# Performance work log

Measured on AMD Instinct MI355X. Metric: run time of the kernel, lower is better.

Reference implementation:

```python
import math
import jax, jax.numpy as jnp
import numpy as np

HEADS = 9
EMBED = 32
TEMPERATURE = 3000.0

def _conv1x1(x, W, b):
    # x: [B,C,H,W], W: [O,C], b: [O]  (1x1 conv == channel matmul)
    return jnp.einsum('bchw,oc->bohw', x, W) + b[None, :, None, None]

def setup_inputs() -> dict:
    key = jax.random.key(0)
    ks = jax.random.split(key, 14)
    B, H, W = 2, 64, 64
    h2, w2 = 32, 32
    hd = HEADS * EMBED  # 288
    s = 0.1
    return {
        'second_frame': jax.random.normal(ks[0], (B, 3, H, W), jnp.float32),
        'first_frame_aligned': jax.random.normal(ks[1], (B, 3, H, W), jnp.float32),
        'second_frame_feat': jax.random.normal(ks[2], (B, 4, h2, w2), jnp.float32),
        'first_frame_feat_aligned': jax.random.normal(ks[3], (B, 4, h2, w2), jnp.float32),
        'Wq': jax.random.normal(ks[4], (hd, 3), jnp.float32) * s,
        'bq': jax.random.normal(ks[5], (hd,), jnp.float32) * s,
        'Wk': jax.random.normal(ks[6], (hd, 3), jnp.float32) * s,
        'bk': jax.random.normal(ks[7], (hd,), jnp.float32) * s,
        'Wv': jax.random.normal(ks[8], (hd, 4), jnp.float32) * s,
        'bv': jax.random.normal(ks[9], (hd,), jnp.float32) * s,
        'Wp': jax.random.normal(ks[10], (4, hd), jnp.float32) * s,
        'bp': jax.random.normal(ks[11], (4,), jnp.float32) * s,
        'Wt': jax.random.normal(ks[12], (1, EMBED), jnp.float32) * s,
        'bt': jax.random.normal(ks[13], (1,), jnp.float32) * s,
    }

def reference(second_frame, first_frame_aligned, second_frame_feat,
              first_frame_feat_aligned, Wq, bq, Wk, bk, Wv, bv, Wp, bp, Wt, bt):
    B, _, H, W = second_frame.shape
    HW = H * W
    # bilinear upsample of aligned features to (H, W); half-pixel centers == align_corners=False
    feat_up = jax.image.resize(first_frame_feat_aligned,
                               (B, first_frame_feat_aligned.shape[1], H, W),
                               method='linear', antialias=False)
    Q = _conv1x1(second_frame, Wq, bq).reshape(B, HEADS, EMBED, HW)
    K = _conv1x1(first_frame_aligned, Wk, bk).reshape(B, HEADS, EMBED, HW)
    V = _conv1x1(feat_up, Wv, bv).reshape(B, HEADS, EMBED, HW)
    Qn = jnp.transpose(Q, (0, 1, 3, 2))                      # [B,h,HW,d]
    sim = jnp.einsum('bhnd,bhdm->bhnm', Qn, K) / math.sqrt(EMBED)  # [B,h,HW,HW]
    # learned per-query threshold from Q
    t = jnp.einsum('bhnd,od->bhno', Qn, Wt) + bt             # [B,h,HW,1]
    attn = jax.nn.relu((sim - t) / TEMPERATURE)              # no row normalization
    out = jnp.einsum('bhnm,bhdm->bhnd', attn, V)             # [B,h,HW,d]
    out = jnp.transpose(out, (0, 1, 3, 2)).reshape(B, HEADS * EMBED, H, W)
    out_feat = _conv1x1(out, Wp, bp)                         # [B,4,H,W]
    h2, w2 = second_frame_feat.shape[-2:]
    out_feat_down = jax.image.resize(out_feat, (B, out_feat.shape[1], h2, w2),
                                     method='linear', antialias=False)
    final_feat = second_frame_feat + out_feat_down
    return final_feat, out_feat_down
```

## Files before the change

kernel.cpp:

```cpp
#include <hip/hip_runtime.h>
#include <hip/hip_bf16.h>
#include <cstddef>

#define NHEADS 9
#define D 32
#define SQ 4096
#define ZSPLIT 4
#define MBLK (SQ / ZSPLIT)
#define CHUNKS (MBLK / 64)
#define KROW 40
#define VROW 70

typedef __attribute__((ext_vector_type(8))) short bf16x8;
typedef __attribute__((ext_vector_type(4))) short bf16x4;
typedef __attribute__((ext_vector_type(4))) float f32x4;

__device__ __forceinline__ unsigned int f2bf(float f) {
    unsigned int u = __float_as_uint(f);
    u += 0x7fffu + ((u >> 16) & 1u);
    return u >> 16;
}

__device__ __forceinline__ unsigned int cvt_pk_bf16(float a, float b) {
#if __has_builtin(__builtin_amdgcn_cvt_pk_bf16_f32)
    typedef __attribute__((ext_vector_type(2))) __bf16 bf2;
    union { bf2 v; unsigned int u; } cv;
    cv.v = __builtin_amdgcn_cvt_pk_bf16_f32(a, b);
    return cv.u;
#else
    return (f2bf(b) << 16) | f2bf(a);
#endif
}

__device__ __forceinline__ bf16x4 relu_pack(f32x4 st) {
    float a0 = fmaxf(st[0], 0.0f);
    float a1 = fmaxf(st[1], 0.0f);
    float a2 = fmaxf(st[2], 0.0f);
    float a3 = fmaxf(st[3], 0.0f);
    union { unsigned int u[2]; bf16x4 v; } r;
    r.u[0] = cvt_pk_bf16(a0, a1);
    r.u[1] = cvt_pk_bf16(a2, a3);
    return r.v;
}

__global__ __launch_bounds__(256) void prep_kernel(
    const float* __restrict__ x2, const float* __restrict__ x1,
    const float* __restrict__ feat1,
    const float* __restrict__ Wq, const float* __restrict__ bq,
    const float* __restrict__ Wk, const float* __restrict__ bk,
    const float* __restrict__ Wv, const float* __restrict__ bv,
    const float* __restrict__ Wt, const float* __restrict__ bt,
    unsigned short* __restrict__ Qb, unsigned short* __restrict__ Kb,
    unsigned short* __restrict__ Vb, float* __restrict__ tbuf,
    float* __restrict__ of)
{
    int idx = blockIdx.x * blockDim.x + threadIdx.x;
    if (idx < 2 * 4 * SQ) of[idx] = 0.0f;
    int g  = idx & 3;
    int n  = (idx >> 2) & (SQ - 1);
    int bh = idx >> 14;
    int h  = bh % NHEADS;
    int b  = bh / NHEADS;

    float xs0 = x2[((size_t)b * 3 + 0) * SQ + n];
    float xs1 = x2[((size_t)b * 3 + 1) * SQ + n];
    float xs2 = x2[((size_t)b * 3 + 2) * SQ + n];
    float ys0 = x1[((size_t)b * 3 + 0) * SQ + n];
    float ys1 = x1[((size_t)b * 3 + 1) * SQ + n];
    float ys2 = x1[((size_t)b * 3 + 2) * SQ + n];

    int yy = n >> 6, xx = n & 63;
    int jy = yy >> 1, jx = xx >> 1;
    int j0, j1, i0, i1; float wy0, wy1, wx0, wx1;
    if (yy & 1) { j0 = jy; j1 = (jy < 31) ? jy + 1 : 31; wy0 = 0.75f; wy1 = 0.25f; }
    else        { j0 = (jy > 0) ? jy - 1 : 0; j1 = jy;   wy0 = 0.25f; wy1 = 0.75f; }
    if (xx & 1) { i0 = jx; i1 = (jx < 31) ? jx + 1 : 31; wx0 = 0.75f; wx1 = 0.25f; }
    else        { i0 = (jx > 0) ? jx - 1 : 0; i1 = jx;   wx0 = 0.25f; wx1 = 0.75f; }

    float fu[4];
#pragma unroll
    for (int c = 0; c < 4; ++c) {
        const float* f = feat1 + ((size_t)b * 4 + c) * 1024;
        fu[c] = wy0 * (wx0 * f[j0 * 32 + i0] + wx1 * f[j0 * 32 + i1]) +
                wy1 * (wx0 * f[j1 * 32 + i0] + wx1 * f[j1 * 32 + i1]);
    }

    const int d0 = g * 8;
    unsigned int qp[4], kp[4], vp[4];
    float tpart = 0.0f;
#pragma unroll
    for (int j = 0; j < 8; ++j) {
        int d = d0 + j, hd = h * D + d;
        float q = bq[hd] + Wq[hd * 3] * xs0 + Wq[hd * 3 + 1] * xs1 + Wq[hd * 3 + 2] * xs2;
        float k = bk[hd] + Wk[hd * 3] * ys0 + Wk[hd * 3 + 1] * ys1 + Wk[hd * 3 + 2] * ys2;
        float v = bv[hd] + Wv[hd * 4] * fu[0] + Wv[hd * 4 + 1] * fu[1] +
                  Wv[hd * 4 + 2] * fu[2] + Wv[hd * 4 + 3] * fu[3];
        tpart += q * Wt[d];
        unsigned int qb_ = f2bf(q), kb_ = f2bf(k), vb_ = f2bf(v);
        if (j & 1) { qp[j >> 1] |= qb_ << 16; kp[j >> 1] |= kb_ << 16; vp[j >> 1] |= vb_ << 16; }
        else       { qp[j >> 1]  = qb_;       kp[j >> 1]  = kb_;       vp[j >> 1]  = vb_; }
    }
    tpart += __shfl_xor(tpart, 1);
    tpart += __shfl_xor(tpart, 2);
    if (g == 0) tbuf[(size_t)bh * SQ + n] = tpart + bt[0];

    size_t base = ((size_t)bh * SQ + n) * D + d0;
    *(uint4*)(Qb + base) = make_uint4(qp[0], qp[1], qp[2], qp[3]);
    *(uint4*)(Kb + base) = make_uint4(kp[0], kp[1], kp[2], kp[3]);
    *(uint4*)(Vb + base) = make_uint4(vp[0], vp[1], vp[2], vp[3]);
}

__global__ __launch_bounds__(256, 4) void attn_kernel(
    const unsigned short* __restrict__ Qb,
    const unsigned short* __restrict__ Kb,
    const unsigned short* __restrict__ Vb,
    const float* __restrict__ tbuf,
    const float* __restrict__ Wp,
    float* __restrict__ of)
{
    __shared__ __align__(16) unsigned short Ks[64 * KROW];
    __shared__ __align__(16) unsigned short Vs[32 * VROW];

    const int bh   = blockIdx.y;
    const int h    = bh % NHEADS;
    const int b    = bh / NHEADS;
    const int n0   = blockIdx.x * 256;
    const int mc0  = blockIdx.z * MBLK;
    const int tid  = threadIdx.x;
    const int wave = tid >> 6;
    const int lane = tid & 63;
    const int l15  = lane & 15;
    const int quad = lane >> 4;

    const int nw = n0 + wave * 64;

    const unsigned short* qbase = Qb + ((size_t)bh * SQ + nw + l15) * D + quad * 8;
    bf16x8 qfA = *(const bf16x8*)(qbase);
    bf16x8 qfB = *(const bf16x8*)(qbase + 16 * D);
    bf16x8 qfC = *(const bf16x8*)(qbase + 32 * D);
    bf16x8 qfD = *(const bf16x8*)(qbase + 48 * D);

    const float SQRT32 = 5.656854249492381f;
    const float* tb = tbuf + (size_t)bh * SQ + nw + l15;
    float TA = tb[0]  * SQRT32;
    float TB = tb[16] * SQRT32;
    float TC = tb[32] * SQRT32;
    float TD = tb[48] * SQRT32;
    const f32x4 ciA = {-TA, -TA, -TA, -TA};
    const f32x4 ciB = {-TB, -TB, -TB, -TB};
    const f32x4 ciC = {-TC, -TC, -TC, -TC};
    const f32x4 ciD = {-TD, -TD, -TD, -TD};

    const uint4* Kg4 = (const uint4*)(Kb + (size_t)bh * SQ * D);
    const uint4* Vg4 = (const uint4*)(Vb + (size_t)bh * SQ * D);

    const int krow = tid >> 2;
    const int kcol = (tid & 3) * 8;
    unsigned short* kdst = Ks + krow * KROW + kcol;
    unsigned short* vdst = Vs + kcol * VROW + krow;

    f32x4 accAl = {0.f,0.f,0.f,0.f}, accAh = {0.f,0.f,0.f,0.f};
    f32x4 accBl = {0.f,0.f,0.f,0.f}, accBh = {0.f,0.f,0.f,0.f};
    f32x4 accCl = {0.f,0.f,0.f,0.f}, accCh = {0.f,0.f,0.f,0.f};
    f32x4 accDl = {0.f,0.f,0.f,0.f}, accDh = {0.f,0.f,0.f,0.f};

    uint4 kreg = Kg4[(size_t)mc0 * 4 + tid];
    uint4 vreg = Vg4[(size_t)mc0 * 4 + tid];

    for (int c = 0; c < CHUNKS; ++c) {
        __syncthreads();
        *(uint4*)kdst = kreg;
        {
            union { uint4 u; unsigned short s[8]; } vv; vv.u = vreg;
#pragma unroll
            for (int j = 0; j < 8; ++j) vdst[j * VROW] = vv.s[j];
        }
        kreg = Kg4[(size_t)(mc0 + (c + 1) * 64) * 4 + tid];
        vreg = Vg4[(size_t)(mc0 + (c + 1) * 64) * 4 + tid];
        __syncthreads();

#pragma unroll
        for (int s = 0; s < 4; ++s) {
            bf16x8 kf = *(const bf16x8*)(Ks + (s * 16 + l15) * KROW + quad * 8);
            bf16x4 va = *(const bf16x4*)(Vs + l15 * VROW + s * 16 + quad * 4);
            bf16x4 vb = *(const bf16x4*)(Vs + (l15 + 16) * VROW + s * 16 + quad * 4);

            f32x4 stA = __builtin_amdgcn_mfma_f32_16x16x32_bf16(kf, qfA, ciA, 0, 0, 0);
            f32x4 stB = __builtin_amdgcn_mfma_f32_16x16x32_bf16(kf, qfB, ciB, 0, 0, 0);
            f32x4 stC = __builtin_amdgcn_mfma_f32_16x16x32_bf16(kf, qfC, ciC, 0, 0, 0);
            f32x4 stD = __builtin_amdgcn_mfma_f32_16x16x32_bf16(kf, qfD, ciD, 0, 0, 0);

            bf16x4 pA = relu_pack(stA);
            bf16x4 pB = relu_pack(stB);
            bf16x4 pC = relu_pack(stC);
            bf16x4 pD = relu_pack(stD);

            accAl = __builtin_amdgcn_mfma_f32_16x16x16bf16_1k(va, pA, accAl, 0, 0, 0);
            accAh = __builtin_amdgcn_mfma_f32_16x16x16bf16_1k(vb, pA, accAh, 0, 0, 0);
            accBl = __builtin_amdgcn_mfma_f32_16x16x16bf16_1k(va, pB, accBl, 0, 0, 0);
            accBh = __builtin_amdgcn_mfma_f32_16x16x16bf16_1k(vb, pB, accBh, 0, 0, 0);
            accCl = __builtin_amdgcn_mfma_f32_16x16x16bf16_1k(va, pC, accCl, 0, 0, 0);
            accCh = __builtin_amdgcn_mfma_f32_16x16x16bf16_1k(vb, pC, accCh, 0, 0, 0);
            accDl = __builtin_amdgcn_mfma_f32_16x16x16bf16_1k(va, pD, accDl, 0, 0, 0);
            accDh = __builtin_amdgcn_mfma_f32_16x16x16bf16_1k(vb, pD, accDh, 0, 0, 0);
        }
    }

    const float s1 = 5.892556509887896e-05f;
    const float* wph = Wp + h * D + quad * 4;
#pragma unroll
    for (int o = 0; o < 4; ++o) {
        float cA = 0.f, cB = 0.f, cC = 0.f, cD = 0.f;
#pragma unroll
        for (int r = 0; r < 4; ++r) {
            float wlo = wph[o * 288 + r], whi = wph[o * 288 + 16 + r];
            cA += accAl[r] * wlo + accAh[r] * whi;
            cB += accBl[r] * wlo + accBh[r] * whi;
            cC += accCl[r] * wlo + accCh[r] * whi;
            cD += accDl[r] * wlo + accDh[r] * whi;
        }
        cA += __shfl_xor(cA, 16); cA += __shfl_xor(cA, 32);
        cB += __shfl_xor(cB, 16); cB += __shfl_xor(cB, 32);
        cC += __shfl_xor(cC, 16); cC += __shfl_xor(cC, 32);
        cD += __shfl_xor(cD, 16); cD += __shfl_xor(cD, 32);
        if (quad == 0) {
            float* ob = &of[((size_t)b * 4 + o) * SQ + nw + l15];
            atomicAdd(ob,      cA * s1);
            atomicAdd(ob + 16, cB * s1);
            atomicAdd(ob + 32, cC * s1);
            atomicAdd(ob + 48, cD * s1);
        }
    }
}

__global__ void final_kernel(const float* __restrict__ of,
                             const float* __restrict__ sff,
                             const float* __restrict__ bp,
                             float* __restrict__ dout)
{
    int tid = blockIdx.x * blockDim.x + threadIdx.x;
    if (tid >= 8192) return;
    int i  = tid & 31;
    int jj = (tid >> 5) & 31;
    int bo = tid >> 10;
    int o  = bo & 3;
    const float* src = of + (size_t)bo * SQ;
    int y = jj * 2, x = i * 2;
    float dval = 0.25f * (src[y * 64 + x] + src[y * 64 + x + 1] +
                          src[(y + 1) * 64 + x] + src[(y + 1) * 64 + x + 1]) + bp[o];
    dout[tid]        = sff[tid] + dval;
    dout[8192 + tid] = dval;
}

extern "C" void kernel_launch(void* const* d_in, const int* in_sizes, int n_in,
                              void* d_out, int out_size, void* d_ws, size_t ws_size,
                              hipStream_t stream)
{
    const float* second_frame = (const float*)d_in[0];
    const float* first_frame  = (const float*)d_in[1];
    const float* sff          = (const float*)d_in[2];
    const float* ffa          = (const float*)d_in[3];
    const float* Wq = (const float*)d_in[4];
    const float* bq = (const float*)d_in[5];
    const float* Wk = (const float*)d_in[6];
    const float* bk = (const float*)d_in[7];
    const float* Wv = (const float*)d_in[8];
    const float* bv = (const float*)d_in[9];
    const float* Wp = (const float*)d_in[10];
    const float* bp = (const float*)d_in[11];
    const float* Wt = (const float*)d_in[12];
    const float* bt = (const float*)d_in[13];
    float* out = (float*)d_out;

    char* ws = (char*)d_ws;
    const size_t QKV = (size_t)2 * NHEADS * SQ * D * sizeof(unsigned short);
    unsigned short* Qb = (unsigned short*)ws;
    unsigned short* Kb = (unsigned short*)(ws + QKV);
    unsigned short* Vb = (unsigned short*)(ws + 2 * QKV);
    float* tbuf = (float*)(ws + 3 * QKV);
    float* of   = (float*)(ws + 3 * QKV + (size_t)2 * NHEADS * SQ * sizeof(float));

    prep_kernel<<<1152, 256, 0, stream>>>(second_frame, first_frame, ffa,
                                          Wq, bq, Wk, bk, Wv, bv, Wt, bt,
                                          Qb, Kb, Vb, tbuf, of);
    dim3 ag(16, 18, ZSPLIT);
    attn_kernel<<<ag, 256, 0, stream>>>(Qb, Kb, Vb, tbuf, Wp, of);
    final_kernel<<<32, 256, 0, stream>>>(of, sff, bp, out);
}
```

Measured before the change: 166.4 us.

## Store V transposed, use 16x16x32 MFMA for PV, and double key split

The prep kernel now writes V as [bh, d, n], so the attention kernel can copy V tiles into shared memory with one 16-byte store instead of eight scalar transposing stores. K rows are placed in a permuted shared-memory layout so that two 16x16x32 score tiles concatenate into an 8-wide P fragment. That lets the PV product use the 16x16x32 bf16 MFMA, halving the PV instruction count. ZSPLIT goes from 4 to 8 to launch more blocks, at the cost of more atomic accumulation into the output, and the prep kernel's V writes become scattered 2-byte stores.

Result: faster. 152.5 us (-8.3%).

```diff
diff --git a/kernel.cpp b/kernel.cpp
--- a/kernel.cpp
+++ b/kernel.cpp
@@ -5,11 +5,11 @@
 #define NHEADS 9
 #define D 32
 #define SQ 4096
-#define ZSPLIT 4
+#define ZSPLIT 8
 #define MBLK (SQ / ZSPLIT)
 #define CHUNKS (MBLK / 64)
 #define KROW 40
-#define VROW 70
+#define VROW 72
 
 typedef __attribute__((ext_vector_type(8))) short bf16x8;
 typedef __attribute__((ext_vector_type(4))) short bf16x4;
@@ -51,7 +51,7 @@
     const float* __restrict__ Wv, const float* __restrict__ bv,
     const float* __restrict__ Wt, const float* __restrict__ bt,
     unsigned short* __restrict__ Qb, unsigned short* __restrict__ Kb,
-    unsigned short* __restrict__ Vb, float* __restrict__ tbuf,
+    unsigned short* __restrict__ Vt, float* __restrict__ tbuf,
     float* __restrict__ of)
 {
     int idx = blockIdx.x * blockDim.x + threadIdx.x;
@@ -86,7 +86,7 @@
     }
 
     const int d0 = g * 8;
-    unsigned int qp[4], kp[4], vp[4];
+    unsigned int qp[4], kp[4];
     float tpart = 0.0f;
 #pragma unroll
     for (int j = 0; j < 8; ++j) {
@@ -96,9 +96,10 @@
         float v = bv[hd] + Wv[hd * 4] * fu[0] + Wv[hd * 4 + 1] * fu[1] +
                   Wv[hd * 4 + 2] * fu[2] + Wv[hd * 4 + 3] * fu[3];
         tpart += q * Wt[d];
-        unsigned int qb_ = f2bf(q), kb_ = f2bf(k), vb_ = f2bf(v);
-        if (j & 1) { qp[j >> 1] |= qb_ << 16; kp[j >> 1] |= kb_ << 16; vp[j >> 1] |= vb_ << 16; }
-        else       { qp[j >> 1]  = qb_;       kp[j >> 1]  = kb_;       vp[j >> 1]  = vb_; }
+        unsigned int qb_ = f2bf(q), kb_ = f2bf(k);
+        if (j & 1) { qp[j >> 1] |= qb_ << 16; kp[j >> 1] |= kb_ << 16; }
+        else       { qp[j >> 1]  = qb_;       kp[j >> 1]  = kb_; }
+        Vt[((size_t)bh * D + d) * SQ + n] = (unsigned short)f2bf(v);
     }
     tpart += __shfl_xor(tpart, 1);
     tpart += __shfl_xor(tpart, 2);
@@ -107,13 +108,12 @@
     size_t base = ((size_t)bh * SQ + n) * D + d0;
     *(uint4*)(Qb + base) = make_uint4(qp[0], qp[1], qp[2], qp[3]);
     *(uint4*)(Kb + base) = make_uint4(kp[0], kp[1], kp[2], kp[3]);
-    *(uint4*)(Vb + base) = make_uint4(vp[0], vp[1], vp[2], vp[3]);
 }
 
 __global__ __launch_bounds__(256, 4) void attn_kernel(
     const unsigned short* __restrict__ Qb,
     const unsigned short* __restrict__ Kb,
-    const unsigned short* __restrict__ Vb,
+    const unsigned short* __restrict__ Vt,
     const float* __restrict__ tbuf,
     const float* __restrict__ Wp,
     float* __restrict__ of)
@@ -152,12 +152,16 @@
     const f32x4 ciD = {-TD, -TD, -TD, -TD};
 
     const uint4* Kg4 = (const uint4*)(Kb + (size_t)bh * SQ * D);
-    const uint4* Vg4 = (const uint4*)(Vb + (size_t)bh * SQ * D);
+    const uint4* Vg4 = (const uint4*)(Vt + (size_t)bh * D * SQ);
 
     const int krow = tid >> 2;
     const int kcol = (tid & 3) * 8;
-    unsigned short* kdst = Ks + krow * KROW + kcol;
-    unsigned short* vdst = Vs + kcol * VROW + krow;
+    const int kslot = (krow & 32) + 4 * ((krow >> 3) & 3) + (krow & 3) + ((krow & 4) << 2);
+    unsigned short* kdst = Ks + kslot * KROW + kcol;
+    const int vd = tid >> 3;
+    const int vm = (tid & 7) * 8;
+    unsigned short* vdst = Vs + vd * VROW + vm;
+    const int vgbase = vd * (SQ / 8) + (mc0 >> 3) + (tid & 7);
 
     f32x4 accAl = {0.f,0.f,0.f,0.f}, accAh = {0.f,0.f,0.f,0.f};
     f32x4 accBl = {0.f,0.f,0.f,0.f}, accBh = {0.f,0.f,0.f,0.f};
@@ -165,44 +169,50 @@
     f32x4 accDl = {0.f,0.f,0.f,0.f}, accDh = {0.f,0.f,0.f,0.f};
 
     uint4 kreg = Kg4[(size_t)mc0 * 4 + tid];
-    uint4 vreg = Vg4[(size_t)mc0 * 4 + tid];
+    uint4 vreg = Vg4[vgbase];
 
     for (int c = 0; c < CHUNKS; ++c) {
         __syncthreads();
         *(uint4*)kdst = kreg;
-        {
-            union { uint4 u; unsigned short s[8]; } vv; vv.u = vreg;
-#pragma unroll
-            for (int j = 0; j < 8; ++j) vdst[j * VROW] = vv.s[j];
-        }
+        *(uint4*)vdst = vreg;
         kreg = Kg4[(size_t)(mc0 + (c + 1) * 64) * 4 + tid];
-        vreg = Vg4[(size_t)(mc0 + (c + 1) * 64) * 4 + tid];
+        vreg = Vg4[vgbase + (c + 1) * 8];
         __syncthreads();
 
 #pragma unroll
-        for (int s = 0; s < 4; ++s) {
-            bf16x8 kf = *(const bf16x8*)(Ks + (s * 16 + l15) * KROW + quad * 8);
-            bf16x4 va = *(const bf16x4*)(Vs + l15 * VROW + s * 16 + quad * 4);
-            bf16x4 vb = *(const bf16x4*)(Vs + (l15 + 16) * VROW + s * 16 + quad * 4);
-
-            f32x4 stA = __builtin_amdgcn_mfma_f32_16x16x32_bf16(kf, qfA, ciA, 0, 0, 0);
-            f32x4 stB = __builtin_amdgcn_mfma_f32_16x16x32_bf16(kf, qfB, ciB, 0, 0, 0);
-            f32x4 stC = __builtin_amdgcn_mfma_f32_16x16x32_bf16(kf, qfC, ciC, 0, 0, 0);
-            f32x4 stD = __builtin_amdgcn_mfma_f32_16x16x32_bf16(kf, qfD, ciD, 0, 0, 0);
-
-            bf16x4 pA = relu_pack(stA);
-            bf16x4 pB = relu_pack(stB);
-            bf16x4 pC = relu_pack(stC);
-            bf16x4 pD = relu_pack(stD);
-
-            accAl = __builtin_amdgcn_mfma_f32_16x16x16bf16_1k(va, pA, accAl, 0, 0, 0);
-            accAh = __builtin_amdgcn_mfma_f32_16x16x16bf16_1k(vb, pA, accAh, 0, 0, 0);
-            accBl = __builtin_amdgcn_mfma_f32_16x16x16bf16_1k(va, pB, accBl, 0, 0, 0);
-            accBh = __builtin_amdgcn_mfma_f32_16x16x16bf16_1k(vb, pB, accBh, 0, 0, 0);
-            accCl = __builtin_amdgcn_mfma_f32_16x16x16bf16_1k(va, pC, accCl, 0, 0, 0);
-            accCh = __builtin_amdgcn_mfma_f32_16x16x16bf16_1k(vb, pC, accCh, 0, 0, 0);
-            accDl = __builtin_amdgcn_mfma_f32_16x16x16bf16_1k(va, pD, accDl, 0, 0, 0);
-            accDh = __builtin_amdgcn_mfma_f32_16x16x16bf16_1k(vb, pD, accDh, 0, 0, 0);
+        for (int g32 = 0; g32 < 2; ++g32) {
+            const unsigned short* kbase = Ks + g32 * 32 * KROW;
+            bf16x8 kf1 = *(const bf16x8*)(kbase + l15 * KROW + quad * 8);
+            bf16x8 kf2 = *(const bf16x8*)(kbase + (16 + l15) * KROW + quad * 8);
+            bf16x8 vlo = *(const bf16x8*)(Vs + l15 * VROW + g32 * 32 + quad * 8);
+            bf16x8 vhi = *(const bf16x8*)(Vs + (l15 + 16) * VROW + g32 * 32 + quad * 8);
+
+            f32x4 sA1 = __builtin_amdgcn_mfma_f32_16x16x32_bf16(kf1, qfA, ciA, 0, 0, 0);
+            f32x4 sA2 = __builtin_amdgcn_mfma_f32_16x16x32_bf16(kf2, qfA, ciA, 0, 0, 0);
+            f32x4 sB1 = __builtin_amdgcn_mfma_f32_16x16x32_bf16(kf1, qfB, ciB, 0, 0, 0);
+            f32x4 sB2 = __builtin_amdgcn_mfma_f32_16x16x32_bf16(kf2, qfB, ciB, 0, 0, 0);
+            f32x4 sC1 = __builtin_amdgcn_mfma_f32_16x16x32_bf16(kf1, qfC, ciC, 0, 0, 0);
+            f32x4 sC2 = __builtin_amdgcn_mfma_f32_16x16x32_bf16(kf2, qfC, ciC, 0, 0, 0);
+            f32x4 sD1 = __builtin_amdgcn_mfma_f32_16x16x32_bf16(kf1, qfD, ciD, 0, 0, 0);
+            f32x4 sD2 = __builtin_amdgcn_mfma_f32_16x16x32_bf16(kf2, qfD, ciD, 0, 0, 0);
+
+            bf16x4 pA1 = relu_pack(sA1), pA2 = relu_pack(sA2);
+            bf16x4 pB1 = relu_pack(sB1), pB2 = relu_pack(sB2);
+            bf16x4 pC1 = relu_pack(sC1), pC2 = relu_pack(sC2);
+            bf16x4 pD1 = relu_pack(sD1), pD2 = relu_pack(sD2);
+            bf16x8 pA = __builtin_shufflevector(pA1, pA2, 0,1,2,3,4,5,6,7);
+            bf16x8 pB = __builtin_shufflevector(pB1, pB2, 0,1,2,3,4,5,6,7);
+            bf16x8 pC = __builtin_shufflevector(pC1, pC2, 0,1,2,3,4,5,6,7);
+            bf16x8 pD = __builtin_shufflevector(pD1, pD2, 0,1,2,3,4,5,6,7);
+
+            accAl = __builtin_amdgcn_mfma_f32_16x16x32_bf16(vlo, pA, accAl, 0, 0, 0);
+            accAh = __builtin_amdgcn_mfma_f32_16x16x32_bf16(vhi, pA, accAh, 0, 0, 0);
+            accBl = __builtin_amdgcn_mfma_f32_16x16x32_bf16(vlo, pB, accBl, 0, 0, 0);
+            accBh = __builtin_amdgcn_mfma_f32_16x16x32_bf16(vhi, pB, accBh, 0, 0, 0);
+            accCl = __builtin_amdgcn_mfma_f32_16x16x32_bf16(vlo, pC, accCl, 0, 0, 0);
+            accCh = __builtin_amdgcn_mfma_f32_16x16x32_bf16(vhi, pC, accCh, 0, 0, 0);
+            accDl = __builtin_amdgcn_mfma_f32_16x16x32_bf16(vlo, pD, accDl, 0, 0, 0);
+            accDh = __builtin_amdgcn_mfma_f32_16x16x32_bf16(vhi, pD, accDh, 0, 0, 0);
         }
     }
 
@@ -276,14 +286,14 @@
     const size_t QKV = (size_t)2 * NHEADS * SQ * D * sizeof(unsigned short);
     unsigned short* Qb = (unsigned short*)ws;
     unsigned short* Kb = (unsigned short*)(ws + QKV);
-    unsigned short* Vb = (unsigned short*)(ws + 2 * QKV);
+    unsigned short* Vt = (unsigned short*)(ws + 2 * QKV);
     float* tbuf = (float*)(ws + 3 * QKV);
     float* of   = (float*)(ws + 3 * QKV + (size_t)2 * NHEADS * SQ * sizeof(float));
 
     prep_kernel<<<1152, 256, 0, stream>>>(second_frame, first_frame, ffa,
                                           Wq, bq, Wk, bk, Wv, bv, Wt, bt,
-                                          Qb, Kb, Vb, tbuf, of);
+                                          Qb, Kb, Vt, tbuf, of);
     dim3 ag(16, 18, ZSPLIT);
-    attn_kernel<<<ag, 256, 0, stream>>>(Qb, Kb, Vb, tbuf, Wp, of);
+    attn_kernel<<<ag, 256, 0, stream>>>(Qb, Kb, Vt, tbuf, Wp, of);
     final_kernel<<<32, 256, 0, stream>>>(of, sff, bp, out);
 }
```
